# Kernel tuning notes

Hardware: AMD Instinct MI355X
Metric: run time of the kernel (lower is better)

## Reference

```python
import jax, jax.numpy as jnp
import numpy as np

B, C, T, H, W = 1, 1, 6, 256, 256
L, F, K, KS = 8, 24, 35, 11
ACT_MIN, ACT_MAX = 0.0, 1.0


def _conv2d(x, w):
    # x: (N,Cin,H,W), w: (Cout,Cin,k,k); 'same' cross-correlation like torch conv2d(padding=k//2)
    return jax.lax.conv_general_dilated(x, w, (1, 1), 'SAME',
                                        dimension_numbers=('NCHW', 'OIHW', 'NCHW'))


def _merge_bt(x):  # (B,Ch,T,H,W) -> (B*T,Ch,H,W): vectorize the per-t python loop
    return x.transpose(0, 2, 1, 3, 4).reshape(-1, x.shape[1], x.shape[3], x.shape[4])


def _split_bt(x, b, t):  # (B*T,Ch,H,W) -> (B,Ch,T,H,W)
    return x.reshape(b, t, x.shape[1], x.shape[2], x.shape[3]).transpose(0, 2, 1, 3, 4)


def _k2i(x):  # centered orthonormal 2D inverse FFT over (H,W)
    return jnp.fft.fftshift(jnp.fft.ifft2(jnp.fft.ifftshift(x, axes=(-2, -1)), norm='ortho'), axes=(-2, -1))


def _i2k(x):  # centered orthonormal 2D FFT over (H,W)
    return jnp.fft.fftshift(jnp.fft.fft2(jnp.fft.ifftshift(x, axes=(-2, -1)), norm='ortho'), axes=(-2, -1))


def _interp(x, kn):
    # fixed-grid piecewise-linear spline: x (B,F,H,W) real, kn (K,F) knot values on [ACT_MIN,ACT_MAX]
    k = kn.shape[0]
    pos = jnp.clip((x - ACT_MIN) * (k - 1) / (ACT_MAX - ACT_MIN), 0.0, k - 1.0)
    idx = jnp.clip(jnp.floor(pos).astype(jnp.int32), 0, k - 2)
    frac = pos - idx
    knT = kn.T  # (F,K)
    ch = jnp.arange(kn.shape[1])[None, :, None, None]
    return knT[ch, idx] * (1.0 - frac) + knT[ch, idx + 1] * frac


def setup_inputs() -> dict:
    key = jax.random.key(0)
    k = jax.random.split(key, 9)
    return {
        'X_ks_real': jax.random.normal(k[0], (B, C, T, H, W), jnp.float32),
        'X_ks_imag': jax.random.normal(k[1], (B, C, T, H, W), jnp.float32),
        'X_mask': (jax.random.uniform(k[2], (B, C, T, 1, W)) > 0.6).astype(jnp.float32),
        'kernels_real': 0.02 * jax.random.normal(k[3], (L, F, C, KS, KS), jnp.float32),
        'kernels_imag': 0.02 * jax.random.normal(k[4], (L, F, C, KS, KS), jnp.float32),
        'knots': 0.1 * jax.random.normal(k[5], (L, K, F), jnp.float32),
        'alphas': 0.1 + 0.9 * jax.random.uniform(k[6], (L,), jnp.float32),
        'momentums': 0.5 * jax.random.uniform(k[7], (L,), jnp.float32),
        'k0': jnp.array(1.0, jnp.float32),
    }


def reference(X_ks_real, X_ks_imag, X_mask, kernels_real, kernels_imag, knots, alphas, momentums, k0):
    X_ks = (X_ks_real + 1j * X_ks_imag).astype(jnp.complex64)
    # normalize_ks_
    norm = jnp.sqrt(jnp.sum(jnp.abs(X_ks) ** 2, axis=(2, 3, 4), keepdims=True)
                    / jnp.sum(X_mask, axis=(2, 3, 4), keepdims=True))
    X_ks = X_ks / norm
    X_img = _k2i(X_ks) * k0
    m = jnp.zeros_like(X_img)
    for l in range(L):
        Dr, Di, kn = kernels_real[l], kernels_imag[l], knots[l]
        # ---- VTV regularizer gradient ----
        xr, xi = _merge_bt(X_img.real), _merge_bt(X_img.imag)
        DXr = _conv2d(xr, Dr) - _conv2d(xi, Di)   # complex conv, real part
        DXi = _conv2d(xr, Di) + _conv2d(xi, Dr)   # complex conv, imag part
        DXr5, DXi5 = _split_bt(DXr, B, T), _split_bt(DXi, B, T)  # (B,F,T,H,W)
        act_in = jnp.sqrt(jnp.sum(DXr5 ** 2 + DXi5 ** 2, axis=2)) / T  # (B,F,H,W)
        act_out = _interp(act_in, kn)[:, :, None]  # (B,F,1,H,W)
        Vr, Vi = _merge_bt(DXr5 * act_out), _merge_bt(DXi5 * act_out)
        # adjoint complex conv: flip spatial, swap in/out channels, conj kernel
        DrT = jnp.flip(Dr, (-2, -1)).transpose(1, 0, 2, 3)
        DiT = jnp.flip(Di, (-2, -1)).transpose(1, 0, 2, 3)
        rg_r = _conv2d(Vr, DrT) + _conv2d(Vi, DiT)
        rg_i = _conv2d(Vi, DrT) - _conv2d(Vr, DiT)
        reg_grad = _split_bt(rg_r, B, T) + 1j * _split_bt(rg_i, B, T)
        # ---- data-consistency gradient ----
        data_grad = _k2i(_i2k(X_img) * X_mask - X_ks)
        grad = alphas[l] * data_grad + reg_grad
        m = momentums[l] * m + grad
        X_img = X_img - m
    X_img = X_img * norm  # denormalize
    return jnp.stack([X_img.real, X_img.imag], axis=-1)  # (B,C,T,H,W,2)
```

## Files before the change

kernel.cpp:

```cpp
#include <hip/hip_runtime.h>
#include <math.h>

#define TT 6
#define FC 24
#define KN 35
#define HW 65536
#define NPIX (TT*HW)
#define CPB 16

#define VSTRIDE 272
#define VROWS   266
#define VPLANE  (VROWS*VSTRIDE)
#define VIOFF   (5*VSTRIDE + 5)
#define NPLANES2 288
#define HALO_PER_PLANE 6816
#define NPARTS 4
#define ADJ_PARTS 4
#define WQ_PER_LAYER (3*11*512)
#define WD_PER_LAYER (24*121*2)

#define AC_ROWS 74
#define AC_F16  48
#define AC_CHNK (AC_ROWS*6)
#define AC_CH2  (2*AC_CHNK)
#define AC_COMP_BYTES (AC_ROWS*AC_F16*2)
#define BFRAG_F16 512
#define BADJ_PER_LAYER_F16 (24*11*2*512)

typedef float v2f __attribute__((ext_vector_type(2)));
typedef float v4f __attribute__((ext_vector_type(4)));
typedef short short8 __attribute__((ext_vector_type(8)));
typedef _Float16 half2_t __attribute__((ext_vector_type(2)));
typedef _Float16 half8_t __attribute__((ext_vector_type(8)));
typedef int  v4i  __attribute__((ext_vector_type(4)));
typedef v4i  v4i_u __attribute__((aligned(4)));

__device__ inline float2 cmulf(float2 a, float2 b){
    return make_float2(a.x*b.x - a.y*b.y, a.x*b.y + a.y*b.x);
}

__device__ inline void gl_lds16(const void* g, void* l){
    __builtin_amdgcn_global_load_lds((const __attribute__((address_space(1))) unsigned int*)g,
                                     (__attribute__((address_space(3))) unsigned int*)l,
                                     16, 0, 0);
}

__device__ __host__ inline unsigned short f2bf(float x){
    unsigned u = __float_as_uint(x);
    unsigned r = (u + 0x7FFFu + ((u >> 16) & 1u)) >> 16;
    return (unsigned short)r;
}

__global__ void halo_zero_kernel(float2* base){
    int gid = blockIdx.x*256 + threadIdx.x;
    if (gid >= TT*HALO_PER_PLANE) return;
    int p = gid / HALO_PER_PLANE;
    int i = gid - p*HALO_PER_PLANE;
    int row, col;
    if (i < 2720){
        row = i / 272; col = i - row*272;
        if (row >= 5) row += 256;
    } else {
        int j = i - 2720;
        row = 5 + j/16;
        col = j & 15;
        if (col >= 5) col += 256;
    }
    base[(long)p*VPLANE + (long)row*VSTRIDE + col] = make_float2(0.f, 0.f);
}

__global__ void halo_zero_vh_kernel(unsigned short* base){
    int gid = blockIdx.x*256 + threadIdx.x;
    if (gid >= NPLANES2*HALO_PER_PLANE) return;
    int p = gid / HALO_PER_PLANE;
    int i = gid - p*HALO_PER_PLANE;
    int row, col;
    if (i < 2720){
        row = i / 272; col = i - row*272;
        if (row >= 5) row += 256;
    } else {
        int j = i - 2720;
        row = 5 + j/16;
        col = j & 15;
        if (col >= 5) col += 256;
    }
    base[(long)p*VPLANE + (long)row*VSTRIDE + col] = 0;
}

__global__ void reduce_kernel(const float* xr, const float* xi, const float* mask, float* sums){
    __shared__ float s1[256], s2[256];
    int tid = threadIdx.x;
    int gid = blockIdx.x*256 + tid;
    float a = 0.f, b = 0.f;
    for (int i = gid; i < NPIX; i += gridDim.x*256) a += xr[i]*xr[i] + xi[i]*xi[i];
    for (int i = gid; i < TT*256; i += gridDim.x*256) b += mask[i];
    s1[tid]=a; s2[tid]=b; __syncthreads();
    for (int off=128; off>0; off>>=1){
        if (tid<off){ s1[tid]+=s1[tid+off]; s2[tid]+=s2[tid+off]; }
        __syncthreads();
    }
    if (tid==0){ atomicAdd(&sums[0], s1[0]); atomicAdd(&sums[1], s2[0]); }
}

__global__ void normalize_kernel(const float* xr, const float* xi, const float* sums, float2* Xks){
    int i = blockIdx.x*256 + threadIdx.x;
    float inv = rsqrtf(sums[0]/sums[1]);
    Xks[i] = make_float2(xr[i]*inv, xi[i]*inv);
}

__global__ void prepack_wfrag_kernel(const float* kr, const float* ki, unsigned short* Wq){
    int idx = blockIdx.x*256 + threadIdx.x;
    if (idx >= 8*WQ_PER_LAYER) return;
    int j    = idx & 7;
    int lane = (idx >> 3) & 63;
    int ky   = (idx >> 9) % 11;
    int nt   = (idx / (512*11)) % 3;
    int l    =  idx / (512*11*3);
    int quad = lane >> 4;
    int k    = quad*8 + j;
    int part = k >> 4;
    int kx   = k & 15;
    int n    = nt*16 + (lane & 15);
    int f    = n >> 1, comp = n & 1;
    float v = 0.f;
    if (kx <= 10){
        long wi = ((long)(l*24+f))*121 + ky*11 + kx;
        float wr = kr[wi], wim = ki[wi];
        v = (comp == 0) ? (part == 0 ? wr  : -wim)
                        : (part == 0 ? wim :  wr );
    }
    Wq[idx] = f2bf(v);
}

__global__ void prepack_badj_kernel(const float* kr, const float* ki, unsigned short* Badj){
    int idx = blockIdx.x*256 + threadIdx.x;
    if (idx >= 8*BADJ_PER_LAYER_F16) return;
    int e    = idx & 511;
    int rest = idx >> 9;
    int comp = rest & 1;
    int ky   = (rest >> 1) % 11;
    int f    = ((rest >> 1) / 11) % 24;
    int l    =  (rest >> 1) / (11*24);
    int lane = e >> 3, j = e & 7;
    int n = lane & 15, q = lane >> 4;
    int kx = 8*q + j - n;
    float v = 0.f;
    if (kx >= 0 && kx <= 10){
        long src = (long)(l*24+f)*121 + (120 - (ky*11 + kx));
        v = comp ? ki[src] : kr[src];
    }
    _Float16 h = (_Float16)v;
    Badj[idx] = *(unsigned short*)&h;
}

__global__ void fft_row_kernel(const float2* __restrict__ in, float2* __restrict__ out,
                               float dir, float scale){
    __shared__ float2 lds[2][256];
    __shared__ float2 tw[128];
    int tid = threadIdx.x;
    int line = tid >> 7;
    int j = tid & 127;
    if (tid < 128){
        float s, c;
        sincosf(dir * 6.283185307179586f * (float)tid / 256.0f, &s, &c);
        tw[tid] = make_float2(c, s);
    }
    long gline = (long)blockIdx.x*2 + line;
    const float2* src = in + gline*256;
    {
        float sg = (j & 1) ? -1.f : 1.f;
        float2 a = src[j];
        float2 b = src[j+128];
        lds[line][j]     = make_float2(a.x*sg, a.y*sg);
        lds[line][j+128] = make_float2(b.x*sg, b.y*sg);
    }
    __syncthreads();
    for (int s = 0; s < 8; s++){
        int half = 128 >> s;
        int pos = j & (half-1);
        int grp = j >> (7-s);
        int i0 = (grp << (8-s)) + pos;
        int i1 = i0 + half;
        float2 u = lds[line][i0], v = lds[line][i1];
        float2 w = tw[pos << s];
        lds[line][i0] = make_float2(u.x+v.x, u.y+v.y);
        float2 d = make_float2(u.x-v.x, u.y-v.y);
        lds[line][i1] = cmulf(d, w);
        __syncthreads();
    }
    float2* dst = out + gline*256;
    {
        int k = j;
        float sg = (k & 1) ? -scale : scale;
        float2 v = lds[line][__brev((unsigned)k) >> 24];
        dst[k] = make_float2(v.x*sg, v.y*sg);
        k = j + 128;
        sg = (k & 1) ? -scale : scale;
        v = lds[line][__brev((unsigned)k) >> 24];
        dst[k] = make_float2(v.x*sg, v.y*sg);
    }
}

__global__ void fft_col_kernel(const float2* __restrict__ in, float2* __restrict__ Xpad,
                               float2* __restrict__ G, unsigned short* __restrict__ Xbf,
                               float dir, float scale, const float* k0){
    __shared__ float2 lds[256][CPB+1];
    __shared__ float2 tw[128];
    int tid = threadIdx.x;
    if (tid < 128){
        float s, c;
        sincosf(dir * 6.283185307179586f * (float)tid / 256.0f, &s, &c);
        tw[tid] = make_float2(c, s);
    }
    int t  = blockIdx.x / (256/CPB);
    int w0 = (blockIdx.x % (256/CPB)) * CPB;
    const float2* src = in + (long)t*HW;
    int c  = tid & (CPB-1);
    int h0 = tid >> 4;
    for (int i = 0; i < 16; i++){
        int h = h0 + 16*i;
        float2 v = src[h*256 + w0 + c];
        float sg = (h & 1) ? -1.f : 1.f;
        lds[h][c] = make_float2(v.x*sg, v.y*sg);
    }
    __syncthreads();
    int jb = tid >> 4;
    for (int s = 0; s < 8; s++){
        int half = 128 >> s;
        for (int i = 0; i < 8; i++){
            int j = jb + 16*i;
            int pos = j & (half-1);
            int grp = j >> (7-s);
            int i0 = (grp << (8-s)) + pos;
            int i1 = i0 + half;
            float2 u = lds[i0][c], v = lds[i1][c];
            float2 w = tw[pos << s];
            lds[i0][c] = make_float2(u.x+v.x, u.y+v.y);
            float2 d = make_float2(u.x-v.x, u.y-v.y);
            lds[i1][c] = cmulf(d, w);
        }
        __syncthreads();
    }
    float kk = *k0;
    for (int i = 0; i < 16; i++){
        int k = h0 + 16*i;
        float2 v = lds[__brev((unsigned)k) >> 24][c];
        float sg = (k & 1) ? -scale : scale;
        float2 g = make_float2(v.x*sg, v.y*sg);
        G[(long)t*HW + k*256 + w0 + c] = g;
        float2 x = make_float2(g.x*kk, g.y*kk);
        long off = VIOFF + (long)k*VSTRIDE + w0 + c;
        Xpad[(long)t*VPLANE + off] = x;
        unsigned short vr = f2bf(x.x), vi = f2bf(x.y);
        Xbf[((long)(0*6+t))*VPLANE + off]     = vr;
        Xbf[((long)(1*6+t))*VPLANE + off]     = vi;
        Xbf[((long)(2*6+t))*VPLANE + off - 1] = vr;
        Xbf[((long)(3*6+t))*VPLANE + off - 1] = vi;
    }
}

__global__ __launch_bounds__(256) void conv_fwd_mfma_kernel(
        const unsigned short* __restrict__ Xbf, const unsigned short* __restrict__ Wq,
        const float* __restrict__ knots, unsigned short* __restrict__ Vp){
    __shared__ __align__(16) unsigned short wlds[WQ_PER_LAYER];
    int tid = threadIdx.x;
    {
        int wv = tid >> 6, ln = tid & 63;
        #pragma unroll
        for (int r = 0; r < 9; r++){
            int c = r*256 + wv*64 + ln;
            if (c < 2112)
                gl_lds16(Wq + (long)c*8, (char*)wlds + (unsigned)(r*256 + wv*64)*16u);
        }
    }
    int h  = blockIdx.y;
    int w0 = blockIdx.x*64;
    int lane = tid & 63, wave = tid >> 6;
    int half = wave >> 1, parity = wave & 1;
    int quad = lane >> 4, l15 = lane & 15;
    int part = quad >> 1, kx0 = (quad & 1)*8;
    int col0 = half*32 + 2*l15 + kx0;

    __syncthreads();

    v4f D[3][6];
    #pragma unroll
    for (int nt = 0; nt < 3; nt++)
        #pragma unroll
        for (int t = 0; t < 6; t++) D[nt][t] = (v4f)(0.f);

    const short8* wl = (const short8*)wlds;
    #pragma unroll
    for (int t = 0; t < 6; t++){
        const unsigned short* ab = Xbf + ((long)((parity*2 + part)*6 + t))*VPLANE
                                       + (long)h*272 + w0 + col0;
        #pragma unroll
        for (int ky = 0; ky < 11; ky++){
            union { v4i i; short8 s; } ua;
            ua.i = *(const v4i_u*)(ab + (long)ky*272);
            short8 a = ua.s;
            #pragma unroll
            for (int nt = 0; nt < 3; nt++){
                short8 b = wl[(nt*11 + ky)*64 + lane];
                D[nt][t] = __builtin_amdgcn_mfma_f32_16x16x32_bf16(a, b, D[nt][t], 0, 0, 0);
            }
        }
    }

    float aout[3][4];
    #pragma unroll
    for (int nt = 0; nt < 3; nt++){
        int f = (nt*16 + l15) >> 1;
        #pragma unroll
        for (int r = 0; r < 4; r++){
            float s = 0.f;
            #pragma unroll
            for (int t = 0; t < 6; t++) s = fmaf(D[nt][t][r], D[nt][t][r], s);
            s += __shfl_xor(s, 1, 64);
            float act_in = sqrtf(s) * (1.0f/6.0f);
            float pos = fminf(fmaxf(act_in * 34.0f, 0.0f), 34.0f);
            int i0 = (int)pos; if (i0 > 33) i0 = 33;
            float frac = pos - (float)i0;
            float k0v = knots[i0*24 + f];
            float k1v = knots[(i0+1)*24 + f];
            aout[nt][r] = k0v*(1.0f - frac) + k1v*frac;
        }
    }

    float* tb = (float*)wlds;
    #pragma unroll
    for (int t = 0; t < 6; t++){
        __syncthreads();
        #pragma unroll
        for (int nt = 0; nt < 3; nt++)
            #pragma unroll
            for (int r = 0; r < 4; r++){
                int px = half*32 + 2*(quad*4 + r) + parity;
                tb[px*50 + nt*16 + l15] = D[nt][t][r] * aout[nt][r];
            }
        __syncthreads();
        #pragma unroll
        for (int q = 0; q < 6; q++){
            int idx = q*256 + tid;
            int f = idx >> 6, px = idx & 63;
            float2 val = *(const float2*)&tb[px*50 + 2*f];
            _Float16 hr = (_Float16)val.x;
            _Float16 hi2 = (_Float16)val.y;
            long off = (long)(t*24 + f)*VPLANE + VIOFF + (long)h*VSTRIDE + (w0 + px);
            Vp[off] = *(unsigned short*)&hr;
            Vp[off + (long)144*VPLANE] = *(unsigned short*)&hi2;
        }
    }
}

__global__ __launch_bounds__(256) void conv_adj_mfma_kernel(
        const unsigned short* __restrict__ Vp, const unsigned short* __restrict__ Badj,
        float2* __restrict__ rg){
    __shared__ __align__(16) unsigned short vt[2][2][AC_ROWS][AC_F16];
    int z = blockIdx.z;
    int t = z % 6, part = z / 6;
    int Y0 = blockIdx.y*64, X0 = blockIdx.x*32;
    int tid = threadIdx.x;
    int w = tid >> 6, l = tid & 63;
    int f0 = part*6;

    const unsigned short* gsrc[4];
    unsigned lofs[4];
    bool act[4];
    {
        const unsigned short* base = Vp + (long)(t*24 + f0)*VPLANE;
        #pragma unroll
        for (int r = 0; r < 4; r++){
            int s = r*256 + tid;
            act[r] = (s < AC_CH2);
            int comp = s / AC_CHNK;
            int rem  = s - comp*AC_CHNK;
            int row  = rem / 6;
            int col  = rem - row*6;
            gsrc[r] = base + (long)comp*144*VPLANE + (long)(Y0 + row)*VSTRIDE + X0 + col*8;
            lofs[r] = (unsigned)(r*256 + w*64)*16u;
        }
    }
    {
        #pragma unroll
        for (int r = 0; r < 4; r++)
            if (act[r]) gl_lds16(gsrc[r], (char*)(&vt[0][0][0][0]) + lofs[r]);
    }

    v4f Drr[2], Dii[2], Dir[2], Dri[2];
    #pragma unroll
    for (int sb = 0; sb < 2; sb++){
        Drr[sb] = (v4f)(0.f); Dii[sb] = (v4f)(0.f);
        Dir[sb] = (v4f)(0.f); Dri[sb] = (v4f)(0.f);
    }

    int m15 = l & 15, q = l >> 4;
    const unsigned short* bgl = Badj + (long)f0*(11*2*BFRAG_F16) + (unsigned)l*8;

    #pragma unroll 1
    for (int k = 0; k < 6; k++){
        int buf = k & 1;
        __syncthreads();
        if (k + 1 < 6){
            #pragma unroll
            for (int r = 0; r < 4; r++){
                if (act[r]) gl_lds16(gsrc[r] + (long)VPLANE, (char*)(&vt[buf^1][0][0][0]) + lofs[r]);
                gsrc[r] += VPLANE;
            }
        }
        const char* va = (const char*)(&vt[buf][0][0][0]) + (w*16 + m15)*96 + q*16;
        const unsigned short* bk = bgl + (long)k*(11*2*BFRAG_F16);
        #pragma unroll
        for (int ky = 0; ky < 11; ky++){
            union { v4i i; half8_t h; } br, bi;
            br.i = *(const v4i*)(bk + ky*(2*BFRAG_F16));
            bi.i = *(const v4i*)(bk + ky*(2*BFRAG_F16) + BFRAG_F16);
            const char* var = va + ky*96;
            #pragma unroll
            for (int sb = 0; sb < 2; sb++){
                union { v4i i; half8_t h; } ar, ai;
                ar.i = *(const v4i*)(var + sb*32);
                ai.i = *(const v4i*)(var + sb*32 + AC_COMP_BYTES);
                Drr[sb] = __builtin_amdgcn_mfma_f32_16x16x32_f16(ar.h, br.h, Drr[sb], 0, 0, 0);
                Dii[sb] = __builtin_amdgcn_mfma_f32_16x16x32_f16(ai.h, bi.h, Dii[sb], 0, 0, 0);
                Dir[sb] = __builtin_amdgcn_mfma_f32_16x16x32_f16(ai.h, br.h, Dir[sb], 0, 0, 0);
                Dri[sb] = __builtin_amdgcn_mfma_f32_16x16x32_f16(ar.h, bi.h, Dri[sb], 0, 0, 0);
            }
        }
    }

    float2* out = rg + (long)part*NPIX + (long)t*HW;
    #pragma unroll
    for (int sb = 0; sb < 2; sb++){
        int x = X0 + 16*sb + m15;
        #pragma unroll
        for (int r = 0; r < 4; r++){
            int y = Y0 + w*16 + q*4 + r;
            out[(long)y*256 + x] = make_float2(Drr[sb][r] + Dii[sb][r],
                                               Dir[sb][r] - Dri[sb][r]);
        }
    }
}

__global__ void dc_update_kernel(float2* __restrict__ Xpad, float2* __restrict__ m,
                                 const float2* __restrict__ rg, const float2* __restrict__ G,
                                 const float* __restrict__ mask, unsigned short* __restrict__ Xbf,
                                 const float* __restrict__ alphas, const float* __restrict__ moms,
                                 int l){
    __shared__ float2 lds[2][256];
    __shared__ float2 tw[128];
    int tid = threadIdx.x;
    int line = tid >> 7;
    int j = tid & 127;
    if (tid < 128){
        float s, c;
        sincosf(6.283185307179586f * (float)tid / 256.0f, &s, &c);
        tw[tid] = make_float2(c, s);
    }
    long gl = (long)blockIdx.x*2 + line;
    int t = (int)(gl >> 8);
    int h = (int)(gl & 255);
    float2* src = Xpad + (long)t*VPLANE + VIOFF + (long)h*VSTRIDE;
    float2 xo0, xo1;
    {
        float sg = (j & 1) ? -1.f : 1.f;
        xo0 = src[j]; xo1 = src[j+128];
        lds[line][j]     = make_float2(xo0.x*sg, xo0.y*sg);
        lds[line][j+128] = make_float2(xo1.x*sg, xo1.y*sg);
    }
    __syncthreads();
    for (int s = 0; s < 8; s++){
        int half = 128 >> s;
        int pos = j & (half-1);
        int grp = j >> (7-s);
        int i0 = (grp << (8-s)) + pos;
        int i1 = i0 + half;
        float2 u = lds[line][i0], v = lds[line][i1];
        float2 w = tw[pos << s]; w.y = -w.y;
        lds[line][i0] = make_float2(u.x+v.x, u.y+v.y);
        float2 d = make_float2(u.x-v.x, u.y-v.y);
        lds[line][i1] = cmulf(d, w);
        __syncthreads();
    }
    {
        int k1 = __brev((unsigned)j) >> 24;
        int k2 = __brev((unsigned)(j+128)) >> 24;
        float mv1 = mask[t*256 + k1] * (1.0f/256.0f);
        float mv2 = mask[t*256 + k2] * (1.0f/256.0f);
        float2 a = lds[line][j], b = lds[line][j+128];
        lds[line][j]     = make_float2(a.x*mv1, a.y*mv1);
        lds[line][j+128] = make_float2(b.x*mv2, b.y*mv2);
    }
    __syncthreads();
    for (int s = 0; s < 8; s++){
        int m2 = 1 << s;
        int pos = j & (m2-1);
        int grp = j >> s;
        int i0 = (grp << (s+1)) + pos;
        int i1 = i0 + m2;
        float2 u = lds[line][i0];
        float2 v = cmulf(lds[line][i1], tw[pos << (7-s)]);
        lds[line][i0] = make_float2(u.x+v.x, u.y+v.y);
        lds[line][i1] = make_float2(u.x-v.x, u.y-v.y);
        __syncthreads();
    }
    float a  = alphas[l];
    float mu = moms[l];
    float sg = (j & 1) ? -1.f : 1.f;
    #pragma unroll
    for (int half = 0; half < 2; half++){
        int k = j + half*128;
        long idx = gl*256 + k;
        float2 d = lds[line][k];
        d = make_float2(d.x*sg, d.y*sg);
        float2 g = G[idx];
        float rx = 0.f, ry = 0.f;
        #pragma unroll
        for (int p = 0; p < ADJ_PARTS; p++){
            float2 r = rg[idx + (long)p*NPIX];
            rx += r.x; ry += r.y;
        }
        float2 grad = make_float2(fmaf(a, d.x - g.x, rx), fmaf(a, d.y - g.y, ry));
        float2 mm;
        if (l == 0){
            mm = grad;
        } else {
            float2 mv = m[idx];
            mm = make_float2(fmaf(mu, mv.x, grad.x), fmaf(mu, mv.y, grad.y));
        }
        m[idx] = mm;
        float2 xo = half ? xo1 : xo0;
        float2 nv = make_float2(xo.x - mm.x, xo.y - mm.y);
        src[k] = nv;
        long off = VIOFF + (long)h*VSTRIDE + k;
        unsigned short vr = f2bf(nv.x), vi = f2bf(nv.y);
        Xbf[((long)(0*6+t))*VPLANE + off]     = vr;
        Xbf[((long)(1*6+t))*VPLANE + off]     = vi;
        Xbf[((long)(2*6+t))*VPLANE + off - 1] = vr;
        Xbf[((long)(3*6+t))*VPLANE + off - 1] = vi;
    }
}

__global__ void output_kernel(const float2* __restrict__ Xpad, const float* __restrict__ sums,
                              float* __restrict__ out){
    int i = blockIdx.x*256 + threadIdx.x;
    int t = i >> 16;
    int p = i & 65535;
    int h = p >> 8, w = p & 255;
    float norm = sqrtf(sums[0]/sums[1]);
    float2 v = Xpad[(long)t*VPLANE + VIOFF + h*VSTRIDE + w];
    out[2*i]   = v.x * norm;
    out[2*i+1] = v.y * norm;
}

extern "C" void kernel_launch(void* const* d_in, const int* in_sizes, int n_in,
                              void* d_out, int out_size, void* d_ws, size_t ws_size,
                              hipStream_t stream){
    const float* Xr    = (const float*)d_in[0];
    const float* Xi    = (const float*)d_in[1];
    const float* mask  = (const float*)d_in[2];
    const float* kr    = (const float*)d_in[3];
    const float* ki    = (const float*)d_in[4];
    const float* knots = (const float*)d_in[5];
    const float* alph  = (const float*)d_in[6];
    const float* moms  = (const float*)d_in[7];
    const float* k0    = (const float*)d_in[8];

    float* ws   = (float*)d_ws;
    float* sums = ws;
    unsigned int*   Wd  = (unsigned int*)(ws + 16);
    unsigned short* Wq  = (unsigned short*)(Wd + 8*WD_PER_LAYER);
    unsigned short* Xbf = Wq + 8*WQ_PER_LAYER;
    float2* mbuf = (float2*)(Xbf + 24*VPLANE);
    float2* G    = mbuf + NPIX;
    float2* rg   = G    + NPIX;
    float2* Xpad = rg   + NPARTS*NPIX;
    unsigned short* Vp = (unsigned short*)(Xpad + TT*VPLANE);
    float2* Xks  = (float2*)Vp;
    unsigned short* Badj = Vp + (size_t)NPLANES2*VPLANE;

    const float OS = 1.0f/16.0f;

    hipMemsetAsync(sums, 0, 2*sizeof(float), stream);
    hipMemsetAsync(Xbf, 0, (size_t)24*VPLANE*sizeof(unsigned short), stream);

    prepack_wfrag_kernel<<<(8*WQ_PER_LAYER + 255)/256, 256, 0, stream>>>(kr, ki, Wq);
    prepack_badj_kernel<<<(8*BADJ_PER_LAYER_F16 + 255)/256, 256, 0, stream>>>(kr, ki, Badj);
    reduce_kernel<<<384, 256, 0, stream>>>(Xr, Xi, mask, sums);
    normalize_kernel<<<NPIX/256, 256, 0, stream>>>(Xr, Xi, sums, Xks);

    fft_row_kernel<<<TT*128, 256, 0, stream>>>(Xks, rg, +1.0f, OS);
    fft_col_kernel<<<TT*(256/CPB), 256, 0, stream>>>(rg, Xpad, G, Xbf, +1.0f, OS, k0);

    halo_zero_kernel<<<(TT*HALO_PER_PLANE + 255)/256, 256, 0, stream>>>(Xpad);
    halo_zero_vh_kernel<<<(NPLANES2*HALO_PER_PLANE + 255)/256, 256, 0, stream>>>(Vp);

    for (int l = 0; l < 8; l++){
        conv_fwd_mfma_kernel<<<dim3(4,256,1), 256, 0, stream>>>(
            Xbf, Wq + (long)l*WQ_PER_LAYER, knots + (long)l*KN*FC, Vp);
        conv_adj_mfma_kernel<<<dim3(8,4,ADJ_PARTS*TT), 256, 0, stream>>>(
            Vp, Badj + (long)l*BADJ_PER_LAYER_F16, rg);
        dc_update_kernel<<<TT*128, 256, 0, stream>>>(Xpad, mbuf, rg, G, mask, Xbf, alph, moms, l);
    }

    output_kernel<<<NPIX/256, 256, 0, stream>>>(Xpad, sums, (float*)d_out);
}
```

Before: 685.4 us.

## Pad adjoint conv LDS rows, remap blocks per XCD, merge halo-zero kernels

Widens the adjoint-conv LDS tile row from 48 to 56 halves (7 chunks per row, 5 load rounds) so the row stride is 112 bytes. The likely intent is to avoid LDS bank conflicts on the MFMA A-fragment reads. The 3D grid becomes a flat 1D grid, remapped so consecutive blocks on the same XCD (bid&7) share a time slice and feature part, which should improve L2 reuse of Vp. Two halo-zeroing kernels are merged into one launch. In exchange the kernel loads more redundant halo data per block.

```diff
diff --git a/kernel.cpp b/kernel.cpp
--- a/kernel.cpp
+++ b/kernel.cpp
@@ -20,10 +20,11 @@
 #define WD_PER_LAYER (24*121*2)
 
 #define AC_ROWS 74
-#define AC_F16  48
-#define AC_CHNK (AC_ROWS*6)
-#define AC_CH2  (2*AC_CHNK)
-#define AC_COMP_BYTES (AC_ROWS*AC_F16*2)
+#define AC_F16  56
+#define AC_CPR  7
+#define AC_CPC  (AC_ROWS*AC_CPR)
+#define AC_CH2  (2*AC_CPC)
+#define AC_COMP_BYTES (AC_CPC*16)
 #define BFRAG_F16 512
 #define BADJ_PER_LAYER_F16 (24*11*2*512)
 
@@ -51,9 +52,9 @@
     return (unsigned short)r;
 }
 
-__global__ void halo_zero_kernel(float2* base){
+__global__ void halo_zero_all_kernel(float2* xpad, unsigned short* vp){
     int gid = blockIdx.x*256 + threadIdx.x;
-    if (gid >= TT*HALO_PER_PLANE) return;
+    if (gid >= (TT + NPLANES2)*HALO_PER_PLANE) return;
     int p = gid / HALO_PER_PLANE;
     int i = gid - p*HALO_PER_PLANE;
     int row, col;
@@ -66,25 +67,12 @@
         col = j & 15;
         if (col >= 5) col += 256;
     }
-    base[(long)p*VPLANE + (long)row*VSTRIDE + col] = make_float2(0.f, 0.f);
-}
-
-__global__ void halo_zero_vh_kernel(unsigned short* base){
-    int gid = blockIdx.x*256 + threadIdx.x;
-    if (gid >= NPLANES2*HALO_PER_PLANE) return;
-    int p = gid / HALO_PER_PLANE;
-    int i = gid - p*HALO_PER_PLANE;
-    int row, col;
-    if (i < 2720){
-        row = i / 272; col = i - row*272;
-        if (row >= 5) row += 256;
+    long off = (long)row*VSTRIDE + col;
+    if (p < TT){
+        xpad[(long)p*VPLANE + off] = make_float2(0.f, 0.f);
     } else {
-        int j = i - 2720;
-        row = 5 + j/16;
-        col = j & 15;
-        if (col >= 5) col += 256;
-    }
-    base[(long)p*VPLANE + (long)row*VSTRIDE + col] = 0;
+        vp[(long)(p - TT)*VPLANE + off] = 0;
+    }
 }
 
 __global__ void reduce_kernel(const float* xr, const float* xi, const float* mask, float* sums){
@@ -356,35 +344,41 @@
 __global__ __launch_bounds__(256) void conv_adj_mfma_kernel(
         const unsigned short* __restrict__ Vp, const unsigned short* __restrict__ Badj,
         float2* __restrict__ rg){
-    __shared__ __align__(16) unsigned short vt[2][2][AC_ROWS][AC_F16];
-    int z = blockIdx.z;
+    __shared__ __align__(16) char vt[2][2*AC_COMP_BYTES];
+    int bid = blockIdx.x;
+    int xcd = bid & 7, bix = bid >> 3;
+    int flat = xcd*96 + bix;
+    int z  = flat >> 5;
+    int r2 = flat & 31;
+    int Y0 = (r2 >> 3) * 64;
+    int X0 = (r2 & 7) * 32;
     int t = z % 6, part = z / 6;
-    int Y0 = blockIdx.y*64, X0 = blockIdx.x*32;
     int tid = threadIdx.x;
     int w = tid >> 6, l = tid & 63;
     int f0 = part*6;
 
-    const unsigned short* gsrc[4];
-    unsigned lofs[4];
-    bool act[4];
+    const unsigned short* gsrc[5];
+    unsigned lofs[5];
+    bool act[5];
     {
         const unsigned short* base = Vp + (long)(t*24 + f0)*VPLANE;
         #pragma unroll
-        for (int r = 0; r < 4; r++){
+        for (int r = 0; r < 5; r++){
             int s = r*256 + tid;
             act[r] = (s < AC_CH2);
-            int comp = s / AC_CHNK;
-            int rem  = s - comp*AC_CHNK;
-            int row  = rem / 6;
-            int col  = rem - row*6;
+            int se = (s < AC_CH2) ? s : (AC_CH2-1);
+            int comp = se / AC_CPC;
+            int rem  = se - comp*AC_CPC;
+            int row  = rem / AC_CPR;
+            int col  = rem - row*AC_CPR;
             gsrc[r] = base + (long)comp*144*VPLANE + (long)(Y0 + row)*VSTRIDE + X0 + col*8;
             lofs[r] = (unsigned)(r*256 + w*64)*16u;
         }
     }
     {
         #pragma unroll
-        for (int r = 0; r < 4; r++)
-            if (act[r]) gl_lds16(gsrc[r], (char*)(&vt[0][0][0][0]) + lofs[r]);
+        for (int r = 0; r < 5; r++)
+            if (act[r]) gl_lds16(gsrc[r], &vt[0][0] + lofs[r]);
     }
 
     v4f Drr[2], Dii[2], Dir[2], Dri[2];
@@ -403,19 +397,19 @@
         __syncthreads();
         if (k + 1 < 6){
             #pragma unroll
-            for (int r = 0; r < 4; r++){
-                if (act[r]) gl_lds16(gsrc[r] + (long)VPLANE, (char*)(&vt[buf^1][0][0][0]) + lofs[r]);
+            for (int r = 0; r < 5; r++){
+                if (act[r]) gl_lds16(gsrc[r] + (long)VPLANE, &vt[buf^1][0] + lofs[r]);
                 gsrc[r] += VPLANE;
             }
         }
-        const char* va = (const char*)(&vt[buf][0][0][0]) + (w*16 + m15)*96 + q*16;
+        const char* va = &vt[buf][0] + (w*16 + m15)*112 + q*16;
         const unsigned short* bk = bgl + (long)k*(11*2*BFRAG_F16);
         #pragma unroll
         for (int ky = 0; ky < 11; ky++){
             union { v4i i; half8_t h; } br, bi;
             br.i = *(const v4i*)(bk + ky*(2*BFRAG_F16));
             bi.i = *(const v4i*)(bk + ky*(2*BFRAG_F16) + BFRAG_F16);
-            const char* var = va + ky*96;
+            const char* var = va + ky*112;
             #pragma unroll
             for (int sb = 0; sb < 2; sb++){
                 union { v4i i; half8_t h; } ar, ai;
@@ -592,13 +586,12 @@
     fft_row_kernel<<<TT*128, 256, 0, stream>>>(Xks, rg, +1.0f, OS);
     fft_col_kernel<<<TT*(256/CPB), 256, 0, stream>>>(rg, Xpad, G, Xbf, +1.0f, OS, k0);
 
-    halo_zero_kernel<<<(TT*HALO_PER_PLANE + 255)/256, 256, 0, stream>>>(Xpad);
-    halo_zero_vh_kernel<<<(NPLANES2*HALO_PER_PLANE + 255)/256, 256, 0, stream>>>(Vp);
+    halo_zero_all_kernel<<<((TT+NPLANES2)*HALO_PER_PLANE + 255)/256, 256, 0, stream>>>(Xpad, Vp);
 
     for (int l = 0; l < 8; l++){
         conv_fwd_mfma_kernel<<<dim3(4,256,1), 256, 0, stream>>>(
             Xbf, Wq + (long)l*WQ_PER_LAYER, knots + (long)l*KN*FC, Vp);
-        conv_adj_mfma_kernel<<<dim3(8,4,ADJ_PARTS*TT), 256, 0, stream>>>(
+        conv_adj_mfma_kernel<<<dim3(8*4*ADJ_PARTS*TT,1,1), 256, 0, stream>>>(
             Vp, Badj + (long)l*BADJ_PER_LAYER_F16, rg);
         dc_update_kernel<<<TT*128, 256, 0, stream>>>(Xpad, mbuf, rg, G, mask, Xbf, alph, moms, l);
     }
```

Measured after the change: 633.9 us. 1.08x faster.
